# Optimization experiments

Measured on AMD Instinct MI355X. Metric: run time of the kernel, lower is better.

The kernel has to match this reference:

```python
import jax, jax.numpy as jnp
import numpy as np
from jax import lax

H = W = 496
K = 5            # gabor kernel size
WIN = 16         # window_size
STRIDE = 16
PATCH = 32
GAMMA = 0.5
PSI = np.pi / 2
THETAS = np.array([np.pi/8, np.pi/4, 3*np.pi/8, np.pi/2, 5*np.pi/8, 6*np.pi/8, 7*np.pi/8, np.pi], dtype=np.float32)


def setup_inputs() -> dict:
    key = jax.random.key(0)
    k1, k2, k3 = jax.random.split(key, 3)
    img = jax.random.normal(k1, (1, 1, H, W), dtype=jnp.float32)
    sigmas = jax.random.uniform(k2, (1, 3), dtype=jnp.float32) * 10.0   # nn.Parameter(rand*10)
    lambdas = jax.random.uniform(k3, (1, 3), dtype=jnp.float32) * np.pi  # nn.Parameter(rand*pi)
    return {"img": img, "sigmas": sigmas, "lambdas": lambdas}


def _gabor_bank(sigmas, lambdas):
    # axes: (sigma, lambda, theta, ky, kx)
    idx = jnp.arange(K, dtype=jnp.float32) - (K - 1) / 2.0
    sig = sigmas[0][:, None, None, None, None]          # [3,1,1,1,1]
    lam = lambdas[0][None, :, None, None, None]         # [1,3,1,1,1]
    th = jnp.asarray(THETAS)[None, None, :, None, None] # [1,1,8,1,1]
    y = idx[None, None, None, :, None]
    x = idx[None, None, None, None, :]
    sigma_x = sig
    sigma_y = sig / GAMMA
    sin_t, cos_t = jnp.sin(th), jnp.cos(th)
    y_theta = -x * sin_t + y * cos_t
    x_theta = x * cos_t + y * sin_t
    gb = jnp.exp(-0.5 * (x_theta**2 / sigma_x**2 + y_theta**2 / sigma_y**2)) \
         * jnp.cos(2.0 * np.pi * x_theta / lam + PSI)
    return gb.reshape(-1, 1, K, K)  # [72,1,5,5]


def reference(img, sigmas, lambdas):
    gb = _gabor_bank(sigmas, lambdas)
    res = lax.conv_general_dilated(
        img, gb, window_strides=(1, 1), padding=[(K // 2, K // 2)] * 2,
        dimension_numbers=("NCHW", "OIHW", "NCHW"))          # [1,72,H,W]
    res = res.reshape(1, 9, 8, H, W).max(axis=2)              # max over 8 thetas -> [1,9,H,W]
    out = res[0]                                              # [9,H,W]

    # find_maxima: per-channel threshold at 5*mean, zero below (torch.nn.Threshold)
    mean = out.mean(axis=(1, 2), keepdims=True)
    thr = jnp.where(out > mean * 5.0, out, 0.0)

    nw = H // STRIDE                                          # 31
    windows = thr.reshape(9, nw, WIN, nw, WIN).transpose(0, 1, 3, 2, 4).reshape(9, nw * nw, WIN * WIN)
    is_max = jnp.argmax(windows, axis=2) == (WIN * WIN) // 2  # [9, 961]

    w_idx = jnp.arange(nw * nw)
    rows = w_idx // nw * STRIDE + WIN // 2
    cols = w_idx % nw * STRIDE + WIN // 2

    # describe: zero-pad by 16, gather 32x32 patch at each candidate keypoint for every channel
    pad = jnp.pad(out, ((0, 0), (16, 16), (16, 16)))
    pr = rows[:, None, None] + jnp.arange(PATCH)[None, :, None]   # [961,32,1]
    pc = cols[:, None, None] + jnp.arange(PATCH)[None, None, :]   # [961,1,32]
    patches = pad[:, pr, pc]                                      # [9,961,32,32]

    # keep patches only for detected keypoints with nonzero content (original skips zero patches)
    valid_kp = jnp.any(is_max, axis=0)                            # [961]
    nonzero = jnp.any(patches != 0, axis=(2, 3))                  # [9,961]
    mask = (valid_kp[None, :] & nonzero).astype(patches.dtype)
    patches = patches * mask[:, :, None, None]
    return patches
```

## Files before the change

kernel.cpp:

```cpp
#include <hip/hip_runtime.h>
#include <math.h>

#define HH 496
#define WW 496
#define HWSZ (HH*WW)
#define NW 31
#define NWIN (NW*NW)

typedef float nf4 __attribute__((ext_vector_type(4)));

__constant__ float c_thetas[8] = {
    0.39269908169872414f, 0.7853981633974483f, 1.1780972450961724f,
    1.5707963267948966f,  1.9634954084936207f, 2.356194490192345f,
    2.748893571891069f,   3.141592653589793f};

__global__ void bank_kernel(const float* __restrict__ sigmas,
                            const float* __restrict__ lambdas,
                            float* __restrict__ filt,
                            float* __restrict__ meanacc) {
    int idx = threadIdx.x + blockIdx.x * blockDim.x;
    if (idx >= 1800) {
        if (idx < 1809) meanacc[(idx - 1800) * 16] = 0.0f;
        return;
    }
    int f = idx / 25, k = idx % 25;
    int dy = k / 5, dx = k % 5;
    int s = f / 24, rem = f % 24, l = rem / 8, t = rem % 8;
    float sig = sigmas[s], lam = lambdas[l], th = c_thetas[t];
    float y = (float)dy - 2.0f, x = (float)dx - 2.0f;
    float st = sinf(th), ct = cosf(th);
    float yt = -x * st + y * ct;
    float xt =  x * ct + y * st;
    float sx2 = sig * sig;
    float sy2 = 4.0f * sig * sig;
    float g = expf(-0.5f * (xt * xt / sx2 + yt * yt / sy2)) *
              cosf(6.28318530717958647692f * xt / lam + 1.5707963267948966f);
    filt[k * 72 + f] = g;
}

#define FMAS(FP, P) \
    a0  = fmaf(P, (FP)[0],  a0);  a1  = fmaf(P, (FP)[1],  a1);  \
    a2  = fmaf(P, (FP)[2],  a2);  a3  = fmaf(P, (FP)[3],  a3);  \
    a4  = fmaf(P, (FP)[4],  a4);  a5  = fmaf(P, (FP)[5],  a5);  \
    a6  = fmaf(P, (FP)[6],  a6);  a7  = fmaf(P, (FP)[7],  a7);  \
    a8  = fmaf(P, (FP)[8],  a8);  a9  = fmaf(P, (FP)[9],  a9);  \
    a10 = fmaf(P, (FP)[10], a10); a11 = fmaf(P, (FP)[11], a11); \
    a12 = fmaf(P, (FP)[12], a12); a13 = fmaf(P, (FP)[13], a13); \
    a14 = fmaf(P, (FP)[14], a14); a15 = fmaf(P, (FP)[15], a15); \
    a16 = fmaf(P, (FP)[16], a16); a17 = fmaf(P, (FP)[17], a17); \
    a18 = fmaf(P, (FP)[18], a18); a19 = fmaf(P, (FP)[19], a19); \
    a20 = fmaf(P, (FP)[20], a20); a21 = fmaf(P, (FP)[21], a21); \
    a22 = fmaf(P, (FP)[22], a22); a23 = fmaf(P, (FP)[23], a23);

#define STEP(K) { const float* fp = fbase + (K)*72; FMAS(fp, p##K) }

#define ALLSTEPS \
    STEP(0)  STEP(1)  STEP(2)  STEP(3)  STEP(4)  \
    STEP(5)  STEP(6)  STEP(7)  STEP(8)  STEP(9)  \
    STEP(10) STEP(11) STEP(12) STEP(13) STEP(14) \
    STEP(15) STEP(16) STEP(17) STEP(18) STEP(19) \
    STEP(20) STEP(21) STEP(22) STEP(23) STEP(24)

__global__ __launch_bounds__(256) void conv_kernel(
    const float* __restrict__ img, const float* __restrict__ filt,
    float* __restrict__ out, float* __restrict__ meanacc) {
    __shared__ float tile[20 * 20];
    __shared__ float red[4][3];
    int tid = threadIdx.x;
    int tx = tid & 15, ty = tid >> 4;
    int bx = blockIdx.x, by = blockIdx.y, cg = blockIdx.z;

    for (int i = tid; i < 400; i += 256) {
        int tY = i / 20, tX = i % 20;
        int gy = by * 16 + tY - 2, gx = bx * 16 + tX - 2;
        float v = 0.0f;
        if (gy >= 0 && gy < HH && gx >= 0 && gx < WW) v = img[gy * WW + gx];
        tile[i] = v;
    }
    __syncthreads();

    int tbase = ty * 20 + tx;
    float p0  = tile[tbase +  0], p1  = tile[tbase +  1], p2  = tile[tbase +  2],
          p3  = tile[tbase +  3], p4  = tile[tbase +  4];
    float p5  = tile[tbase + 20], p6  = tile[tbase + 21], p7  = tile[tbase + 22],
          p8  = tile[tbase + 23], p9  = tile[tbase + 24];
    float p10 = tile[tbase + 40], p11 = tile[tbase + 41], p12 = tile[tbase + 42],
          p13 = tile[tbase + 43], p14 = tile[tbase + 44];
    float p15 = tile[tbase + 60], p16 = tile[tbase + 61], p17 = tile[tbase + 62],
          p18 = tile[tbase + 63], p19 = tile[tbase + 64];
    float p20 = tile[tbase + 80], p21 = tile[tbase + 81], p22 = tile[tbase + 82],
          p23 = tile[tbase + 83], p24 = tile[tbase + 84];

    float a0=0,a1=0,a2=0,a3=0,a4=0,a5=0,a6=0,a7=0,a8=0,a9=0,a10=0,a11=0,
          a12=0,a13=0,a14=0,a15=0,a16=0,a17=0,a18=0,a19=0,a20=0,a21=0,a22=0,a23=0;
    const float* fbase = filt + cg * 24;

    ALLSTEPS

    int y = by * 16 + ty, x = bx * 16 + tx;

    float m0 = fmaxf(fmaxf(fmaxf(a0,a1),fmaxf(a2,a3)),fmaxf(fmaxf(a4,a5),fmaxf(a6,a7)));
    float m1 = fmaxf(fmaxf(fmaxf(a8,a9),fmaxf(a10,a11)),fmaxf(fmaxf(a12,a13),fmaxf(a14,a15)));
    float m2 = fmaxf(fmaxf(fmaxf(a16,a17),fmaxf(a18,a19)),fmaxf(fmaxf(a20,a21),fmaxf(a22,a23)));

    out[(cg * 3 + 0) * HWSZ + y * WW + x] = m0;
    out[(cg * 3 + 1) * HWSZ + y * WW + x] = m1;
    out[(cg * 3 + 2) * HWSZ + y * WW + x] = m2;

#define RED(CC, MV) { \
        float s = MV; \
        s += __shfl_down(s, 32, 64); s += __shfl_down(s, 16, 64); \
        s += __shfl_down(s,  8, 64); s += __shfl_down(s,  4, 64); \
        s += __shfl_down(s,  2, 64); s += __shfl_down(s,  1, 64); \
        if ((tid & 63) == 0) red[tid >> 6][CC] = s; }
    RED(0, m0) RED(1, m1) RED(2, m2)
    __syncthreads();
    if (tid < 3)
        atomicAdd(&meanacc[(cg * 3 + tid) * 16],
                  red[0][tid] + red[1][tid] + red[2][tid] + red[3][tid]);
}

__global__ __launch_bounds__(256) void patch_kernel(
    const float* __restrict__ out, const float* __restrict__ meanacc,
    float* __restrict__ dst) {
    int w = blockIdx.x;
    int r = w / NW, cl = w % NW;
    int tid = threadIdx.x;
    __shared__ int lds_and[4];
    __shared__ int lds_or[4];

    int wy = tid >> 4, wx = tid & 15;
    int rowbase = (r * 16 + wy) * WW + cl * 16 + wx;
    int cbase   = (r * 16 + 8) * WW + cl * 16;
    int okmask = 0;
#pragma unroll
    for (int c = 0; c < 9; c++) {
        float m5 = meanacc[c * 16] * (5.0f / (float)HWSZ);
        float v  = out[c * HWSZ + rowbase];
        float vc = out[c * HWSZ + cbase];
        float thr  = (v  > m5) ? v  : 0.0f;
        float thrc = (vc > m5) ? vc : 0.0f;
        bool ok = (tid < 128) ? (thr < thrc) : (thr <= thrc);
        okmask |= (ok ? 1 : 0) << c;
    }
#pragma unroll
    for (int off = 1; off < 64; off <<= 1) okmask &= __shfl_xor(okmask, off, 64);
    if ((tid & 63) == 0) lds_and[tid >> 6] = okmask;

    int i = tid >> 3;
    int jg = (tid & 7) << 2;
    int row = r * 16 + i - 8;
    int col = cl * 16 + jg - 8;
    bool inb = (row >= 0 && row < HH && col >= 0 && col + 3 < WW);
    size_t pbase = (size_t)row * WW + col;
    int nzmask = 0;
    nf4 p0, p1, p2, p3, p4, p5, p6, p7, p8;
#define LOADP(C, V) { \
        V = (nf4){0.f, 0.f, 0.f, 0.f}; \
        if (inb) V = *(const nf4*)(out + (size_t)(C) * HWSZ + pbase); \
        if (V.x != 0.f || V.y != 0.f || V.z != 0.f || V.w != 0.f) nzmask |= 1 << (C); }
    LOADP(0,p0) LOADP(1,p1) LOADP(2,p2) LOADP(3,p3) LOADP(4,p4)
    LOADP(5,p5) LOADP(6,p6) LOADP(7,p7) LOADP(8,p8)

#pragma unroll
    for (int off = 1; off < 64; off <<= 1) nzmask |= __shfl_xor(nzmask, off, 64);
    if ((tid & 63) == 0) lds_or[tid >> 6] = nzmask;
    __syncthreads();

    int am = lds_and[0] & lds_and[1] & lds_and[2] & lds_and[3];
    int om = lds_or[0] | lds_or[1] | lds_or[2] | lds_or[3];
    bool valid = (am != 0);

    size_t dbase = (size_t)w * 1024 + i * 32 + jg;
#define STOREP(C, V) { \
        float mk = (valid && ((om >> (C)) & 1)) ? 1.0f : 0.0f; \
        V *= mk; \
        __builtin_nontemporal_store(V, (nf4*)(dst + (size_t)(C) * NWIN * 1024 + dbase)); }
    STOREP(0,p0) STOREP(1,p1) STOREP(2,p2) STOREP(3,p3) STOREP(4,p4)
    STOREP(5,p5) STOREP(6,p6) STOREP(7,p7) STOREP(8,p8)
}

extern "C" void kernel_launch(void* const* d_in, const int* in_sizes, int n_in,
                              void* d_out, int out_size, void* d_ws, size_t ws_size,
                              hipStream_t stream) {
    const float* img     = (const float*)d_in[0];
    const float* sigmas  = (const float*)d_in[1];
    const float* lambdas = (const float*)d_in[2];
    float* ws = (float*)d_ws;
    float* filt    = ws;
    float* meanacc = ws + 2048;
    float* outb    = ws + 4096;

    bank_kernel<<<8, 256, 0, stream>>>(sigmas, lambdas, filt, meanacc);
    conv_kernel<<<dim3(NW, NW, 3), 256, 0, stream>>>(img, filt, outb, meanacc);
    patch_kernel<<<NWIN, 256, 0, stream>>>(outb, meanacc, (float*)d_out);
}
```

Before: 122.7 us.

## Loop channel groups per block, replace atomics with partial sums, early-exit invalid windows

The conv kernel now loops over the three channel groups inside one block, so the image tile is loaded once and the grid shrinks to 961 blocks. Per-block partial sums go to a workspace array instead of being combined with atomicAdd into zeroed accumulators, and each patch block reduces those 961 partials itself to get the channel means. The patch kernel also checks the window-max condition first and, for windows that fail it, writes zeros without loading the patch data. The cost is redundant mean reductions in every patch block and less parallelism in the conv kernel.

```diff
diff --git a/kernel.cpp b/kernel.cpp
--- a/kernel.cpp
+++ b/kernel.cpp
@@ -6,6 +6,7 @@
 #define HWSZ (HH*WW)
 #define NW 31
 #define NWIN (NW*NW)
+#define PARTSTRIDE 1024
 
 typedef float nf4 __attribute__((ext_vector_type(4)));
 
@@ -16,13 +17,9 @@
 
 __global__ void bank_kernel(const float* __restrict__ sigmas,
                             const float* __restrict__ lambdas,
-                            float* __restrict__ filt,
-                            float* __restrict__ meanacc) {
+                            float* __restrict__ filt) {
     int idx = threadIdx.x + blockIdx.x * blockDim.x;
-    if (idx >= 1800) {
-        if (idx < 1809) meanacc[(idx - 1800) * 16] = 0.0f;
-        return;
-    }
+    if (idx >= 1800) return;
     int f = idx / 25, k = idx % 25;
     int dy = k / 5, dx = k % 5;
     int s = f / 24, rem = f % 24, l = rem / 8, t = rem % 8;
@@ -61,14 +58,21 @@
     STEP(15) STEP(16) STEP(17) STEP(18) STEP(19) \
     STEP(20) STEP(21) STEP(22) STEP(23) STEP(24)
 
+#define RED(CC, MV) { \
+        float s_ = MV; \
+        s_ += __shfl_down(s_, 32, 64); s_ += __shfl_down(s_, 16, 64); \
+        s_ += __shfl_down(s_,  8, 64); s_ += __shfl_down(s_,  4, 64); \
+        s_ += __shfl_down(s_,  2, 64); s_ += __shfl_down(s_,  1, 64); \
+        if ((tid & 63) == 0) red[tid >> 6][CC] = s_; }
+
 __global__ __launch_bounds__(256) void conv_kernel(
     const float* __restrict__ img, const float* __restrict__ filt,
-    float* __restrict__ out, float* __restrict__ meanacc) {
+    float* __restrict__ out, float* __restrict__ partial) {
     __shared__ float tile[20 * 20];
-    __shared__ float red[4][3];
+    __shared__ float red[4][9];
     int tid = threadIdx.x;
     int tx = tid & 15, ty = tid >> 4;
-    int bx = blockIdx.x, by = blockIdx.y, cg = blockIdx.z;
+    int bx = blockIdx.x, by = blockIdx.y;
 
     for (int i = tid; i < 400; i += 256) {
         int tY = i / 20, tX = i % 20;
@@ -91,43 +95,59 @@
     float p20 = tile[tbase + 80], p21 = tile[tbase + 81], p22 = tile[tbase + 82],
           p23 = tile[tbase + 83], p24 = tile[tbase + 84];
 
-    float a0=0,a1=0,a2=0,a3=0,a4=0,a5=0,a6=0,a7=0,a8=0,a9=0,a10=0,a11=0,
-          a12=0,a13=0,a14=0,a15=0,a16=0,a17=0,a18=0,a19=0,a20=0,a21=0,a22=0,a23=0;
-    const float* fbase = filt + cg * 24;
-
-    ALLSTEPS
-
     int y = by * 16 + ty, x = bx * 16 + tx;
 
-    float m0 = fmaxf(fmaxf(fmaxf(a0,a1),fmaxf(a2,a3)),fmaxf(fmaxf(a4,a5),fmaxf(a6,a7)));
-    float m1 = fmaxf(fmaxf(fmaxf(a8,a9),fmaxf(a10,a11)),fmaxf(fmaxf(a12,a13),fmaxf(a14,a15)));
-    float m2 = fmaxf(fmaxf(fmaxf(a16,a17),fmaxf(a18,a19)),fmaxf(fmaxf(a20,a21),fmaxf(a22,a23)));
-
-    out[(cg * 3 + 0) * HWSZ + y * WW + x] = m0;
-    out[(cg * 3 + 1) * HWSZ + y * WW + x] = m1;
-    out[(cg * 3 + 2) * HWSZ + y * WW + x] = m2;
-
-#define RED(CC, MV) { \
-        float s = MV; \
-        s += __shfl_down(s, 32, 64); s += __shfl_down(s, 16, 64); \
-        s += __shfl_down(s,  8, 64); s += __shfl_down(s,  4, 64); \
-        s += __shfl_down(s,  2, 64); s += __shfl_down(s,  1, 64); \
-        if ((tid & 63) == 0) red[tid >> 6][CC] = s; }
-    RED(0, m0) RED(1, m1) RED(2, m2)
-    __syncthreads();
-    if (tid < 3)
-        atomicAdd(&meanacc[(cg * 3 + tid) * 16],
-                  red[0][tid] + red[1][tid] + red[2][tid] + red[3][tid]);
+#pragma unroll 1
+    for (int cg = 0; cg < 3; ++cg) {
+        const float* fbase = filt + cg * 24;
+        float a0=0,a1=0,a2=0,a3=0,a4=0,a5=0,a6=0,a7=0,a8=0,a9=0,a10=0,a11=0,
+              a12=0,a13=0,a14=0,a15=0,a16=0,a17=0,a18=0,a19=0,a20=0,a21=0,a22=0,a23=0;
+
+        ALLSTEPS
+
+        float m0 = fmaxf(fmaxf(fmaxf(a0,a1),fmaxf(a2,a3)),fmaxf(fmaxf(a4,a5),fmaxf(a6,a7)));
+        float m1 = fmaxf(fmaxf(fmaxf(a8,a9),fmaxf(a10,a11)),fmaxf(fmaxf(a12,a13),fmaxf(a14,a15)));
+        float m2 = fmaxf(fmaxf(fmaxf(a16,a17),fmaxf(a18,a19)),fmaxf(fmaxf(a20,a21),fmaxf(a22,a23)));
+
+        out[(cg * 3 + 0) * HWSZ + y * WW + x] = m0;
+        out[(cg * 3 + 1) * HWSZ + y * WW + x] = m1;
+        out[(cg * 3 + 2) * HWSZ + y * WW + x] = m2;
+
+        RED(cg * 3 + 0, m0)
+        RED(cg * 3 + 1, m1)
+        RED(cg * 3 + 2, m2)
+    }
+
+    __syncthreads();
+    if (tid < 9) {
+        int bid = by * NW + bx;
+        partial[tid * PARTSTRIDE + bid] =
+            red[0][tid] + red[1][tid] + red[2][tid] + red[3][tid];
+    }
 }
 
 __global__ __launch_bounds__(256) void patch_kernel(
-    const float* __restrict__ out, const float* __restrict__ meanacc,
+    const float* __restrict__ out, const float* __restrict__ partial,
     float* __restrict__ dst) {
     int w = blockIdx.x;
     int r = w / NW, cl = w % NW;
     int tid = threadIdx.x;
+    __shared__ float sm5[9];
     __shared__ int lds_and[4];
     __shared__ int lds_or[4];
+
+    {
+        int lane = tid & 63, wid = tid >> 6;
+        for (int c = wid; c < 9; c += 4) {
+            float s = 0.0f;
+            for (int b = lane; b < NWIN; b += 64) s += partial[c * PARTSTRIDE + b];
+            s += __shfl_down(s, 32, 64); s += __shfl_down(s, 16, 64);
+            s += __shfl_down(s,  8, 64); s += __shfl_down(s,  4, 64);
+            s += __shfl_down(s,  2, 64); s += __shfl_down(s,  1, 64);
+            if (lane == 0) sm5[c] = s * (5.0f / (float)HWSZ);
+        }
+    }
+    __syncthreads();
 
     int wy = tid >> 4, wx = tid & 15;
     int rowbase = (r * 16 + wy) * WW + cl * 16 + wx;
@@ -135,7 +155,7 @@
     int okmask = 0;
 #pragma unroll
     for (int c = 0; c < 9; c++) {
-        float m5 = meanacc[c * 16] * (5.0f / (float)HWSZ);
+        float m5 = sm5[c];
         float v  = out[c * HWSZ + rowbase];
         float vc = out[c * HWSZ + cbase];
         float thr  = (v  > m5) ? v  : 0.0f;
@@ -146,9 +166,22 @@
 #pragma unroll
     for (int off = 1; off < 64; off <<= 1) okmask &= __shfl_xor(okmask, off, 64);
     if ((tid & 63) == 0) lds_and[tid >> 6] = okmask;
+    __syncthreads();
+
+    int am = lds_and[0] & lds_and[1] & lds_and[2] & lds_and[3];
 
     int i = tid >> 3;
     int jg = (tid & 7) << 2;
+    size_t dbase = (size_t)w * 1024 + i * 32 + jg;
+
+    if (am == 0) {
+        nf4 z = (nf4){0.f, 0.f, 0.f, 0.f};
+#pragma unroll
+        for (int c = 0; c < 9; c++)
+            __builtin_nontemporal_store(z, (nf4*)(dst + (size_t)c * NWIN * 1024 + dbase));
+        return;
+    }
+
     int row = r * 16 + i - 8;
     int col = cl * 16 + jg - 8;
     bool inb = (row >= 0 && row < HH && col >= 0 && col + 3 < WW);
@@ -167,13 +200,10 @@
     if ((tid & 63) == 0) lds_or[tid >> 6] = nzmask;
     __syncthreads();
 
-    int am = lds_and[0] & lds_and[1] & lds_and[2] & lds_and[3];
     int om = lds_or[0] | lds_or[1] | lds_or[2] | lds_or[3];
-    bool valid = (am != 0);
-
-    size_t dbase = (size_t)w * 1024 + i * 32 + jg;
+
 #define STOREP(C, V) { \
-        float mk = (valid && ((om >> (C)) & 1)) ? 1.0f : 0.0f; \
+        float mk = ((om >> (C)) & 1) ? 1.0f : 0.0f; \
         V *= mk; \
         __builtin_nontemporal_store(V, (nf4*)(dst + (size_t)(C) * NWIN * 1024 + dbase)); }
     STOREP(0,p0) STOREP(1,p1) STOREP(2,p2) STOREP(3,p3) STOREP(4,p4)
@@ -188,10 +218,10 @@
     const float* lambdas = (const float*)d_in[2];
     float* ws = (float*)d_ws;
     float* filt    = ws;
-    float* meanacc = ws + 2048;
-    float* outb    = ws + 4096;
-
-    bank_kernel<<<8, 256, 0, stream>>>(sigmas, lambdas, filt, meanacc);
-    conv_kernel<<<dim3(NW, NW, 3), 256, 0, stream>>>(img, filt, outb, meanacc);
-    patch_kernel<<<NWIN, 256, 0, stream>>>(outb, meanacc, (float*)d_out);
-}
+    float* partial = ws + 2048;
+    float* outb    = ws + 16384;
+
+    bank_kernel<<<8, 256, 0, stream>>>(sigmas, lambdas, filt);
+    conv_kernel<<<dim3(NW, NW), 256, 0, stream>>>(img, filt, outb, partial);
+    patch_kernel<<<NWIN, 256, 0, stream>>>(outb, partial, (float*)d_out);
+}
```

After: 119.9 us. 2.3% less time.
